# Optimization experiments

Measured on AMD Instinct MI355X. Metric: run time of the kernel, lower is better.

## Reference

```python
import jax, jax.numpy as jnp
import numpy as np

D_MODEL = 1024
N_HEADS = 16
HEAD_DIM = D_MODEL // N_HEADS
D_FF = 4 * D_MODEL
B, T = 2, 2048
EPS = 1e-5


def setup_inputs() -> dict:
    key = jax.random.key(0)
    ks = jax.random.split(key, 12)
    s = 0.02
    x = jax.random.normal(ks[0], (B, T, D_MODEL), dtype=jnp.float32)
    # causal mask: True where attention is disallowed (masked_fill semantics)
    mask = jnp.triu(jnp.ones((T, T), dtype=bool), k=1)[None, None]
    def lin(k, out_d, in_d):
        return jax.random.normal(k, (out_d, in_d), dtype=jnp.float32) * s
    return {
        "x": x,
        "mask": mask,
        "wq_w": lin(ks[1], D_MODEL, D_MODEL), "wq_b": jnp.zeros((D_MODEL,), jnp.float32),
        "wk_w": lin(ks[2], D_MODEL, D_MODEL), "wk_b": jnp.zeros((D_MODEL,), jnp.float32),
        "wv_w": lin(ks[3], D_MODEL, D_MODEL), "wv_b": jnp.zeros((D_MODEL,), jnp.float32),
        "wo_w": lin(ks[4], D_MODEL, D_MODEL), "wo_b": jnp.zeros((D_MODEL,), jnp.float32),
        "fc1_w": lin(ks[5], D_FF, D_MODEL), "fc1_b": jnp.zeros((D_FF,), jnp.float32),
        "fc2_w": lin(ks[6], D_MODEL, D_FF), "fc2_b": jnp.zeros((D_MODEL,), jnp.float32),
        "ln1_g": jnp.ones((D_MODEL,), jnp.float32), "ln1_b": jnp.zeros((D_MODEL,), jnp.float32),
        "ln2_g": jnp.ones((D_MODEL,), jnp.float32), "ln2_b": jnp.zeros((D_MODEL,), jnp.float32),
    }


def _layer_norm(x, g, b):
    mu = jnp.mean(x, axis=-1, keepdims=True)
    var = jnp.mean(jnp.square(x - mu), axis=-1, keepdims=True)
    return (x - mu) * jax.lax.rsqrt(var + EPS) * g + b


def reference(x, mask, wq_w, wq_b, wk_w, wk_b, wv_w, wv_b, wo_w, wo_b,
              fc1_w, fc1_b, fc2_w, fc2_b, ln1_g, ln1_b, ln2_g, ln2_b):
    Bx, Tx, C = x.shape
    # --- attention sub-block (pre-norm) ---
    h = _layer_norm(x, ln1_g, ln1_b)
    q = h @ wq_w.T + wq_b
    k = h @ wk_w.T + wk_b
    v = h @ wv_w.T + wv_b
    # split heads: [B,T,C] -> [B,H,T,Dh]
    def split(t):
        return t.reshape(Bx, Tx, N_HEADS, HEAD_DIM).transpose(0, 2, 1, 3)
    q, k, v = split(q), split(k), split(v)
    scores = jnp.einsum('bhqd,bhkd->bhqk', q, k) / jnp.sqrt(jnp.float32(HEAD_DIM))
    scores = jnp.where(mask, jnp.float32(-1e9), scores)
    attn = jax.nn.softmax(scores, axis=-1)
    ctx = jnp.einsum('bhqk,bhkd->bhqd', attn, v)
    ctx = ctx.transpose(0, 2, 1, 3).reshape(Bx, Tx, C)
    x = x + (ctx @ wo_w.T + wo_b)
    # --- FFN sub-block (pre-norm) ---
    h = _layer_norm(x, ln2_g, ln2_b)
    h = jax.nn.gelu(h @ fc1_w.T + fc1_b, approximate=False)
    x = x + (h @ fc2_w.T + fc2_b)
    return x
```

## Files before the change

### kernel.cpp

```cpp
#include <hip/hip_runtime.h>
#include <stdint.h>

typedef unsigned short u16;
typedef __bf16 bf16x8 __attribute__((ext_vector_type(8)));
typedef float floatx4 __attribute__((ext_vector_type(4)));

#define AS1(p) ((__attribute__((address_space(1))) void*)(void*)(p))
#define AS3(p) ((__attribute__((address_space(3))) void*)(p))

__device__ __forceinline__ u16 f2bf(float f) {
    unsigned u;
    __builtin_memcpy(&u, &f, 4);
    u += 0x7FFF + ((u >> 16) & 1);
    return (u16)(u >> 16);
}
__device__ __forceinline__ u16 f2bf_trunc(float f) {
    unsigned u;
    __builtin_memcpy(&u, &f, 4);
    return (u16)(u >> 16);
}
__device__ __forceinline__ float exp2_fast(float x) {
    return __builtin_amdgcn_exp2f(x);
}
__device__ __forceinline__ float gelu_f(float x) {
    return 0.5f * x * (1.0f + erff(x * 0.70710678118654752f));
}

__global__ __launch_bounds__(256) void conv_w_kernel(
    const float* __restrict__ wq, const float* __restrict__ wk,
    const float* __restrict__ wv, const float* __restrict__ wo,
    const float* __restrict__ f1, const float* __restrict__ f2,
    const float* __restrict__ bq, const float* __restrict__ bk,
    const float* __restrict__ bv, float* __restrict__ qkvb,
    u16* __restrict__ W) {
    const size_t i4 = ((size_t)blockIdx.x * 256 + threadIdx.x) * 4;
    const size_t M1 = 1048576;
    const float* src;
    size_t off;
    if (i4 < M1)            { src = wq; off = i4; }
    else if (i4 < 2 * M1)   { src = wk; off = i4 - M1; }
    else if (i4 < 3 * M1)   { src = wv; off = i4 - 2 * M1; }
    else if (i4 < 4 * M1)   { src = wo; off = i4 - 3 * M1; }
    else if (i4 < 8 * M1)   { src = f1; off = i4 - 4 * M1; }
    else                    { src = f2; off = i4 - 8 * M1; }
    float4 d = *(const float4*)(src + off);
    ushort4 o;
    o.x = f2bf(d.x); o.y = f2bf(d.y); o.z = f2bf(d.z); o.w = f2bf(d.w);
    *(ushort4*)(W + i4) = o;
    if (blockIdx.x == 0) {
        for (int i = threadIdx.x; i < 1024; i += 256) {
            qkvb[i] = bq[i];
            qkvb[1024 + i] = bk[i];
            qkvb[2048 + i] = bv[i];
        }
    }
}

__global__ __launch_bounds__(64) void ln_kernel(const float* __restrict__ X,
                                                const float* __restrict__ G,
                                                const float* __restrict__ Bt,
                                                u16* __restrict__ Y) {
    const int row = blockIdx.x;
    const int lane = threadIdx.x;
    const float* xr = X + (size_t)row * 1024;
    float v[16];
    float s = 0.f;
#pragma unroll
    for (int i = 0; i < 16; ++i) { v[i] = xr[lane + i * 64]; s += v[i]; }
#pragma unroll
    for (int off = 1; off < 64; off <<= 1) s += __shfl_xor(s, off, 64);
    const float mu = s * (1.0f / 1024.0f);
    float ss = 0.f;
#pragma unroll
    for (int i = 0; i < 16; ++i) { float d = v[i] - mu; ss += d * d; }
#pragma unroll
    for (int off = 1; off < 64; off <<= 1) ss += __shfl_xor(ss, off, 64);
    const float rstd = rsqrtf(ss * (1.0f / 1024.0f) + 1e-5f);
    u16* yr = Y + (size_t)row * 1024;
#pragma unroll
    for (int i = 0; i < 16; ++i) {
        int c = lane + i * 64;
        yr[c] = f2bf((v[i] - mu) * rstd * G[c] + Bt[c]);
    }
}

__global__ __launch_bounds__(256, 3) void gemm128_kernel(
    const u16* __restrict__ A, const u16* __restrict__ Bt,
    const float* __restrict__ bias, const float* __restrict__ resid,
    float* __restrict__ C, int M, int N, int K) {
    __shared__ __align__(16) u16 lA[2 * 128 * 64];
    __shared__ __align__(16) u16 lB[2 * 64 * 64];
    const int tid = threadIdx.x;
    const int wave = tid >> 6, lane = tid & 63;
    const int wm = (wave >> 1) * 64;
    const int wn = (wave & 1) * 32;
    const int lr = lane & 15, lk8 = (lane >> 4) * 8;
    const int r0 = (lane >> 4) * 4;
    const int m0 = blockIdx.x * 128, n0 = blockIdx.y * 64;
    const int NT = K >> 6;
    const u16* const Ab = A + (size_t)m0 * K;
    const u16* const Bb = Bt + (size_t)n0 * K;

    const int srow = tid >> 3;
    const int scol = 8 * ((tid & 7) ^ (srow & 7));
    const int sdst = tid * 8;
    const int swz = (lr & 7) << 3;
    const int c0 = lk8 ^ swz;
    const int c1 = (32 + lk8) ^ swz;

    floatx4 acc[4][2];
#pragma unroll
    for (int i = 0; i < 4; ++i)
#pragma unroll
        for (int j = 0; j < 2; ++j) acc[i][j] = floatx4{0.f, 0.f, 0.f, 0.f};
    bf16x8 aF[4][2], bF[2][2];

#define STAGE128(Pb, Tt)                                                       \
    {                                                                          \
        _Pragma("unroll")                                                      \
        for (int l = 0; l < 4; ++l) {                                          \
            const u16* srcA = Ab + (size_t)(l * 32 + srow) * K +               \
                              (size_t)(Tt) * 64 + scol;                        \
            __builtin_amdgcn_global_load_lds(                                  \
                AS1(srcA), AS3(lA + (Pb) * 8192 + l * 2048 + sdst), 16, 0, 0); \
        }                                                                      \
        _Pragma("unroll")                                                      \
        for (int l = 0; l < 2; ++l) {                                          \
            const u16* srcB = Bb + (size_t)(l * 32 + srow) * K +               \
                              (size_t)(Tt) * 64 + scol;                        \
            __builtin_amdgcn_global_load_lds(                                  \
                AS1(srcB), AS3(lB + (Pb) * 4096 + l * 2048 + sdst), 16, 0, 0); \
        }                                                                      \
    }
#define GROUP128(P, T)                                                         \
    {                                                                          \
        if ((T) + 1 < NT) {                                                    \
            STAGE128((P) ^ 1, (T) + 1);                                        \
            asm volatile("s_waitcnt vmcnt(6)" ::: "memory");                   \
        } else {                                                               \
            asm volatile("s_waitcnt vmcnt(0)" ::: "memory");                   \
        }                                                                      \
        asm volatile("s_barrier" ::: "memory");                                \
        _Pragma("unroll")                                                      \
        for (int i = 0; i < 4; ++i) {                                          \
            aF[i][0] = *(const bf16x8*)&lA[(P) * 8192 + (wm + i * 16 + lr) * 64 + c0]; \
            aF[i][1] = *(const bf16x8*)&lA[(P) * 8192 + (wm + i * 16 + lr) * 64 + c1]; \
        }                                                                      \
        _Pragma("unroll")                                                      \
        for (int j = 0; j < 2; ++j) {                                          \
            bF[j][0] = *(const bf16x8*)&lB[(P) * 4096 + (wn + j * 16 + lr) * 64 + c0]; \
            bF[j][1] = *(const bf16x8*)&lB[(P) * 4096 + (wn + j * 16 + lr) * 64 + c1]; \
        }                                                                      \
        asm volatile("s_waitcnt lgkmcnt(0)" ::: "memory");                     \
        __builtin_amdgcn_sched_barrier(0);                                     \
        __builtin_amdgcn_s_setprio(1);                                         \
        _Pragma("unroll")                                                      \
        for (int i = 0; i < 4; ++i)                                            \
            _Pragma("unroll")                                                  \
            for (int j = 0; j < 2; ++j)                                        \
                _Pragma("unroll")                                              \
                for (int kk = 0; kk < 2; ++kk)                                 \
                    acc[i][j] = __builtin_amdgcn_mfma_f32_16x16x32_bf16(       \
                        aF[i][kk], bF[j][kk], acc[i][j], 0, 0, 0);             \
        __builtin_amdgcn_s_setprio(0);                                         \
        asm volatile("s_barrier" ::: "memory");                                \
    }

    STAGE128(0, 0);
    for (int T = 0; T < NT; T += 2) {
        GROUP128(0, T);
        GROUP128(1, T + 1);
    }
#undef GROUP128
#undef STAGE128

#pragma unroll
    for (int i = 0; i < 4; ++i)
#pragma unroll
        for (int j = 0; j < 2; ++j) {
            const int col = n0 + wn + j * 16 + lr;
            const float bv = bias[col];
#pragma unroll
            for (int r = 0; r < 4; ++r) {
                const int row = m0 + wm + i * 16 + r0 + r;
                C[(size_t)row * N + col] =
                    acc[i][j][r] + bv + resid[(size_t)row * N + col];
            }
        }
}

__global__ __launch_bounds__(512, 2) void gemm256_kernel(
    const u16* __restrict__ A, const u16* __restrict__ Bt,
    const float* __restrict__ bias, u16* __restrict__ C,
    int M, int N, int K, int act) {
    extern __shared__ __align__(16) u16 smem[];
    u16* const lA = smem;
    u16* const lB = smem + 32768;
    const int tid = threadIdx.x;
    const int wave = tid >> 6, lane = tid & 63;
    const int wm = (wave >> 2) * 128;
    const int wn = (wave & 3) * 64;
    const int lr = lane & 15, lk8 = (lane >> 4) * 8;
    const int r0 = (lane >> 4) * 4;

    const int gM = M >> 8;
    int bid = blockIdx.x;
    { const int nwg = gridDim.x;
      const int q = nwg >> 3, r = nwg & 7, xcd = bid & 7, lid = bid >> 3;
      bid = (xcd < r ? xcd * (q + 1) : r * (q + 1) + (xcd - r) * q) + lid; }
    const int m0 = (bid % gM) << 8;
    const int n0 = (bid / gM) << 8;

    const int NT = K >> 6;
    const u16* const Ab = A + (size_t)m0 * K;
    const u16* const Bb = Bt + (size_t)n0 * K;

    const int srow = tid >> 3;
    const int scol = 8 * ((tid & 7) ^ (srow & 7));
    const int sdst = tid * 8;
    const int swz = (lr & 7) << 3;
    const int c0 = lk8 ^ swz;
    const int c1 = (32 + lk8) ^ swz;

    floatx4 acc[8][4];
#pragma unroll
    for (int i = 0; i < 8; ++i)
#pragma unroll
        for (int j = 0; j < 4; ++j) acc[i][j] = floatx4{0.f, 0.f, 0.f, 0.f};
    bf16x8 aF[2][4][2];
    bf16x8 bF[4][2];

#define STAGE_HT(ldsbuf, gbase, h, Tt)                                         \
    {                                                                          \
        _Pragma("unroll")                                                      \
        for (int l = 0; l < 2; ++l) {                                          \
            const u16* src = (gbase) + (size_t)((h) * 128 + l * 64 + srow) * K \
                             + (size_t)(Tt) * 64 + scol;                       \
            __builtin_amdgcn_global_load_lds(                                  \
                AS1(src), AS3((ldsbuf) + (h) * 8192 + l * 4096 + sdst), 16, 0, 0); \
        }                                                                      \
    }
#define PH_BAR() asm volatile("s_barrier" ::: "memory")
#define LGKM0()                                                                \
    do { asm volatile("s_waitcnt lgkmcnt(0)" ::: "memory");                    \
         __builtin_amdgcn_sched_barrier(0); } while (0)
#define MFMA_Q(mq, nq)                                                         \
    __builtin_amdgcn_s_setprio(1);                                             \
    _Pragma("unroll")                                                          \
    for (int i = 0; i < 4; ++i)                                                \
        _Pragma("unroll")                                                      \
        for (int j = 0; j < 2; ++j)                                            \
            _Pragma("unroll")                                                  \
            for (int kk = 0; kk < 2; ++kk)                                     \
                acc[(mq) * 4 + i][(nq) * 2 + j] =                              \
                    __builtin_amdgcn_mfma_f32_16x16x32_bf16(                   \
                        aF[mq][i][kk], bF[(nq) * 2 + j][kk],                   \
                        acc[(mq) * 4 + i][(nq) * 2 + j], 0, 0, 0);             \
    __builtin_amdgcn_s_setprio(0);

#define GROUP(P, T)                                                            \
    {                                                                          \
        u16* const lAp = lA + (P) * 16384;                                     \
        u16* const lBp = lB + (P) * 16384;                                     \
        u16* const lBn = lB + ((P) ^ 1) * 16384;                               \
                                                                  \
        _Pragma("unroll")                                                      \
        for (int i = 0; i < 4; ++i) {                                          \
            aF[0][i][0] = *(const bf16x8*)&lAp[(wm + i * 16 + lr) * 64 + c0];  \
            aF[0][i][1] = *(const bf16x8*)&lAp[(wm + i * 16 + lr) * 64 + c1];  \
        }                                                                      \
        _Pragma("unroll")                                                      \
        for (int nf = 0; nf < 4; ++nf) {                                       \
            bF[nf][0] = *(const bf16x8*)&lBp[(wn + nf * 16 + lr) * 64 + c0];   \
            bF[nf][1] = *(const bf16x8*)&lBp[(wn + nf * 16 + lr) * 64 + c1];   \
        }                                                                      \
        if ((T) + 1 < NT) STAGE_HT(lBn, Bb, 0, (T) + 1);                       \
        PH_BAR(); LGKM0();                                                     \
        MFMA_Q(0, 0);                                                          \
        PH_BAR();                                                              \
                                                                  \
        _Pragma("unroll")                                                      \
        for (int i = 0; i < 4; ++i) {                                          \
            aF[1][i][0] = *(const bf16x8*)&lAp[(wm + 64 + i * 16 + lr) * 64 + c0]; \
            aF[1][i][1] = *(const bf16x8*)&lAp[(wm + 64 + i * 16 + lr) * 64 + c1]; \
        }                                                                      \
        if ((T) + 1 < NT) STAGE_HT(lBn, Bb, 1, (T) + 1);                       \
        PH_BAR(); LGKM0();                                                     \
        MFMA_Q(0, 1);                                                          \
        PH_BAR();                                                              \
             \
        if ((T) + 2 < NT) STAGE_HT(lAp, Ab, 0, (T) + 2);                       \
        MFMA_Q(1, 0);                                                          \
                                                                  \
        if ((T) + 2 < NT) STAGE_HT(lAp, Ab, 1, (T) + 2);                       \
        MFMA_Q(1, 1);                                                          \
        if ((T) + 2 < NT) asm volatile("s_waitcnt vmcnt(4)" ::: "memory");     \
        else              asm volatile("s_waitcnt vmcnt(0)" ::: "memory");     \
        PH_BAR();                                                              \
    }

    STAGE_HT(lA, Ab, 0, 0);
    STAGE_HT(lA, Ab, 1, 0);
    STAGE_HT(lB, Bb, 0, 0);
    STAGE_HT(lB, Bb, 1, 0);
    if (NT > 1) {
        STAGE_HT(lA + 16384, Ab, 0, 1);
        STAGE_HT(lA + 16384, Ab, 1, 1);
    }
    asm volatile("s_waitcnt vmcnt(4)" ::: "memory");
    PH_BAR();

    for (int T = 0; T < NT; T += 2) {
        GROUP(0, T);
        GROUP(1, T + 1);
    }
#undef GROUP
#undef MFMA_Q
#undef LGKM0
#undef PH_BAR
#undef STAGE_HT

#pragma unroll
    for (int mq = 0; mq < 2; ++mq)
#pragma unroll
        for (int i = 0; i < 4; ++i)
#pragma unroll
            for (int nf = 0; nf < 4; ++nf) {
                const int col = n0 + wn + nf * 16 + lr;
                const float bv = bias[col];
                floatx4 v = acc[mq * 4 + i][nf];
#pragma unroll
                for (int r = 0; r < 4; ++r) {
                    const int row = m0 + wm + mq * 64 + i * 16 + r0 + r;
                    float x = v[r] + bv;
                    if (act) x = gelu_f(x);
                    C[(size_t)row * N + col] = f2bf(x);
                }
            }
}

__global__ __launch_bounds__(256) void transp_v(const u16* __restrict__ qkv,
                                                u16* __restrict__ vT) {
    __shared__ u16 lT[64 * 64];
    const int bh = blockIdx.x, tt = blockIdx.y;
    const int b = bh >> 4, h = bh & 15;
    const int t0 = tt * 64;
    const int tid = threadIdx.x;
    const int srow = tid >> 3, scol = (tid & 7) * 8;
#pragma unroll
    for (int rr = 0; rr < 2; ++rr) {
        const int row = srow + rr * 32;
        uint4 d4 = *(const uint4*)(qkv + (size_t)(b * 2048 + t0 + row) * 3072 +
                                   2048 + h * 64 + scol);
        const u16* e = (const u16*)&d4;
#pragma unroll
        for (int t = 0; t < 8; ++t) lT[(scol + t) * 64 + row] = e[t];
    }
    __syncthreads();
#pragma unroll
    for (int rr = 0; rr < 2; ++rr) {
        const int row = srow + rr * 32;
        uint4 d4 = *(const uint4*)&lT[row * 64 + scol];
        *(uint4*)(vT + (size_t)(bh * 64 + row) * 2048 + t0 + scol) = d4;
    }
}

__global__ __launch_bounds__(256) void attn_kernel(const u16* __restrict__ qkv,
                                                   const u16* __restrict__ vT,
                                                   u16* __restrict__ O) {
    __shared__ __align__(16) u16 lK[2][64 * 64];
    __shared__ __align__(16) u16 lV[2][64 * 64];
    __shared__ __align__(16) u16 lP[4][16 * 64];
    const int tid = threadIdx.x;
    const int wave = tid >> 6, lane = tid & 63;
    const int lr = lane & 15, khi = lane >> 4, lk8 = khi * 8;
    const int p = blockIdx.x;
    const int bh = blockIdx.y;
    const int b = bh >> 4, hh = bh & 15;
    const int rb = b * 2048;
    const size_t vbase = (size_t)(bh * 64) * 2048;
    const int r0 = khi * 4;
    const int qa = 31 - p, qb = p;
    const int qa0 = qa * 64, qb0 = qb * 64;
    const float C = 0.125f * 1.44269504088896f;

    const int srow = tid >> 3;
    const int scol = 8 * ((tid & 7) ^ (srow & 7));
    const int sdst = tid * 8;
    const int swz = (lr & 7) << 3;
    const int cc0 = lk8 ^ swz;
    const int cc1 = (32 + lk8) ^ swz;

    bf16x8 aqA0, aqA1, aqB0, aqB1;
    {
        const size_t qoffA = (size_t)(rb + qa0 + wave * 16 + lr) * 3072 + hh * 64;
        aqA0 = *(const bf16x8*)(qkv + qoffA + lk8);
        aqA1 = *(const bf16x8*)(qkv + qoffA + 32 + lk8);
        const size_t qoffB = (size_t)(rb + qb0 + wave * 16 + lr) * 3072 + hh * 64;
        aqB0 = *(const bf16x8*)(qkv + qoffB + lk8);
        aqB1 = *(const bf16x8*)(qkv + qoffB + 32 + lk8);
    }

    floatx4 oA[4], oB[4];
    float lA_[4], lB_[4];
#pragma unroll
    for (int r = 0; r < 4; ++r) {
        oA[r] = floatx4{0.f, 0.f, 0.f, 0.f};
        oB[r] = floatx4{0.f, 0.f, 0.f, 0.f};
        lA_[r] = 0.f; lB_[r] = 0.f;
    }

#define ASTAGE(Pb, kt_)                                                        \
    {                                                                          \
        const int k0_ = (kt_) * 64;                                            \
        _Pragma("unroll")                                                      \
        for (int rr = 0; rr < 2; ++rr) {                                       \
            const int row = srow + rr * 32;                                    \
            __builtin_amdgcn_global_load_lds(                                  \
                AS1(qkv + (size_t)(rb + k0_ + row) * 3072 + 1024 + hh * 64 + scol), \
                AS3(lK[Pb] + rr * 2048 + sdst), 16, 0, 0);                     \
            __builtin_amdgcn_global_load_lds(                                  \
                AS1(vT + vbase + (size_t)row * 2048 + k0_ + scol),             \
                AS3(lV[Pb] + rr * 2048 + sdst), 16, 0, 0);                     \
        }                                                                      \
    }

#define TILE_ROUND(Pb, aq0_, aq1_, oo_, ll_, q0_, diag_, k0_)                   \
    {                                                                           \
        float s[4][4];                                                          \
        __builtin_amdgcn_s_setprio(1);                                          \
        _Pragma("unroll")                                                       \
        for (int j = 0; j < 4; ++j) {                                           \
            bf16x8 bk0 = *(const bf16x8*)&lK[Pb][(j * 16 + lr) * 64 + cc0];     \
            bf16x8 bk1 = *(const bf16x8*)&lK[Pb][(j * 16 + lr) * 64 + cc1];     \
            floatx4 t = floatx4{0.f, 0.f, 0.f, 0.f};                            \
            t = __builtin_amdgcn_mfma_f32_16x16x32_bf16(aq0_, bk0, t, 0, 0, 0); \
            t = __builtin_amdgcn_mfma_f32_16x16x32_bf16(aq1_, bk1, t, 0, 0, 0); \
            _Pragma("unroll")                                                   \
            for (int r = 0; r < 4; ++r) s[j][r] = t[r];                         \
        }                                                                       \
        __builtin_amdgcn_s_setprio(0);                                          \
        if (diag_) {                                                            \
            _Pragma("unroll")                                                   \
            for (int j = 0; j < 4; ++j)                                         \
                _Pragma("unroll")                                               \
                for (int r = 0; r < 4; ++r)                                     \
                    if ((k0_) + j * 16 + lr > (q0_) + wave * 16 + r0 + r)       \
                        s[j][r] = -1e30f;                                       \
        }                                                                       \
        _Pragma("unroll")                                                       \
        for (int j = 0; j < 4; ++j)                                             \
            _Pragma("unroll")                                                   \
            for (int r = 0; r < 4; ++r) {                                       \
                float pv = exp2_fast(s[j][r] * C);                              \
                ll_[r] += pv;                                                   \
                lP[wave][(r0 + r) * 64 +                                        \
                         ((j * 16 + lr) ^ (((r0 + r) & 7) << 3))] =             \
                    f2bf_trunc(pv);                                             \
            }                                                                   \
        bf16x8 ap0 = *(const bf16x8*)&lP[wave][lr * 64 + cc0];                  \
        bf16x8 ap1 = *(const bf16x8*)&lP[wave][lr * 64 + cc1];                  \
        __builtin_amdgcn_s_setprio(1);                                          \
        _Pragma("unroll")                                                       \
        for (int jd = 0; jd < 4; ++jd) {                                        \
            bf16x8 bv0 = *(const bf16x8*)&lV[Pb][(jd * 16 + lr) * 64 + cc0];    \
            bf16x8 bv1 = *(const bf16x8*)&lV[Pb][(jd * 16 + lr) * 64 + cc1];    \
            oo_[jd] = __builtin_amdgcn_mfma_f32_16x16x32_bf16(ap0, bv0, oo_[jd], 0, 0, 0); \
            oo_[jd] = __builtin_amdgcn_mfma_f32_16x16x32_bf16(ap1, bv1, oo_[jd], 0, 0, 0); \
        }                                                                       \
        __builtin_amdgcn_s_setprio(0);                                          \
    }

    ASTAGE(0, 0);
    for (int kt = 0; kt <= qa; ++kt) {
        const int P = kt & 1;
        const int k0 = kt * 64;
        if (kt < qa) {
            ASTAGE(P ^ 1, kt + 1);
            asm volatile("s_waitcnt vmcnt(4)" ::: "memory");
        } else {
            asm volatile("s_waitcnt vmcnt(0)" ::: "memory");
        }
        asm volatile("s_barrier" ::: "memory");

        TILE_ROUND(P, aqA0, aqA1, oA, lA_, qa0, kt == qa, k0);
        if (kt <= qb)
            TILE_ROUND(P, aqB0, aqB1, oB, lB_, qb0, kt == qb, k0);

        asm volatile("s_barrier" ::: "memory");
    }
#undef TILE_ROUND
#undef ASTAGE

#pragma unroll
    for (int off = 1; off < 16; off <<= 1)
#pragma unroll
        for (int r = 0; r < 4; ++r) {
            lA_[r] += __shfl_xor(lA_[r], off, 64);
            lB_[r] += __shfl_xor(lB_[r], off, 64);
        }

#pragma unroll
    for (int r = 0; r < 4; ++r) {
        const float invA = 1.0f / lA_[r];
        const float invB = 1.0f / lB_[r];
#pragma unroll
        for (int jd = 0; jd < 4; ++jd) {
            const size_t offA = (size_t)(rb + qa0 + wave * 16 + r0 + r) * 1024 +
                                hh * 64 + jd * 16 + lr;
            O[offA] = f2bf(oA[jd][r] * invA);
            const size_t offB = (size_t)(rb + qb0 + wave * 16 + r0 + r) * 1024 +
                                hh * 64 + jd * 16 + lr;
            O[offB] = f2bf(oB[jd][r] * invB);
        }
    }
}

extern "C" void kernel_launch(void* const* d_in, const int* in_sizes, int n_in,
                              void* d_out, int out_size, void* d_ws, size_t ws_size,
                              hipStream_t stream) {
    const float* x     = (const float*)d_in[0];
    const float* wq_w  = (const float*)d_in[2];
    const float* wq_b  = (const float*)d_in[3];
    const float* wk_w  = (const float*)d_in[4];
    const float* wk_b  = (const float*)d_in[5];
    const float* wv_w  = (const float*)d_in[6];
    const float* wv_b  = (const float*)d_in[7];
    const float* wo_w  = (const float*)d_in[8];
    const float* wo_b  = (const float*)d_in[9];
    const float* fc1_w = (const float*)d_in[10];
    const float* fc1_b = (const float*)d_in[11];
    const float* fc2_w = (const float*)d_in[12];
    const float* fc2_b = (const float*)d_in[13];
    const float* ln1_g = (const float*)d_in[14];
    const float* ln1_b = (const float*)d_in[15];
    const float* ln2_g = (const float*)d_in[16];
    const float* ln2_b = (const float*)d_in[17];
    float* out = (float*)d_out;

    char* ws = (char*)d_ws;
    const size_t M1 = 1048576;
    const size_t MB = 1048576;
    u16* Wc    = (u16*)ws;
    u16* wqc   = Wc;
    u16* woc   = Wc + 3 * M1;
    u16* f1c   = Wc + 4 * M1;
    u16* f2c   = Wc + 8 * M1;
    u16* h     = (u16*)(ws + 24 * MB);
    u16* ctx   = h;
    u16* qkv   = (u16*)(ws + 32 * MB);
    u16* vT    = (u16*)(ws + 56 * MB);
    u16* ffh   = (u16*)(ws + 32 * MB);
    float* x1  = (float*)(ws + 64 * MB);
    float* qkvb = x1;
    u16* h2    = h;

    const dim3 blk(256);

    static bool s_attr_done = false;
    if (!s_attr_done) {
        hipFuncSetAttribute(reinterpret_cast<const void*>(gemm256_kernel),
                            hipFuncAttributeMaxDynamicSharedMemorySize, 131072);
        s_attr_done = true;
    }

    conv_w_kernel<<<12288, 256, 0, stream>>>(wq_w, wk_w, wv_w, wo_w, fc1_w, fc2_w,
                                             wq_b, wk_b, wv_b, qkvb, Wc);
    ln_kernel<<<4096, 64, 0, stream>>>(x, ln1_g, ln1_b, h);
    gemm256_kernel<<<dim3(16 * 12), dim3(512), 131072, stream>>>(
        h, wqc, qkvb, qkv, 4096, 3072, 1024, 0);
    transp_v<<<dim3(32, 32), blk, 0, stream>>>(qkv, vT);
    attn_kernel<<<dim3(16, 32), blk, 0, stream>>>(qkv, vT, ctx);
    gemm128_kernel<<<dim3(32, 16), blk, 0, stream>>>(
        ctx, woc, wo_b, x, x1, 4096, 1024, 1024);
    ln_kernel<<<4096, 64, 0, stream>>>(x1, ln2_g, ln2_b, h2);
    gemm256_kernel<<<dim3(16 * 16), dim3(512), 131072, stream>>>(
        h2, f1c, fc1_b, ffh, 4096, 4096, 1024, 1);
    gemm128_kernel<<<dim3(32, 16), blk, 0, stream>>>(
        ffh, f2c, fc2_b, x1, out, 4096, 1024, 4096);
}
```

Before: 360.6 us.

## Widen output-projection GEMMs to 128x128 tiles with a 4-stage LDS pipeline

Replaces the 128x64 residual GEMM with a 128x128 tile that keeps four K-stages in dynamic shared memory, so loads are prefetched three iterations ahead and each iteration needs one barrier instead of two. Each wave now computes a 64x64 sub-tile, which raises MFMA work per LDS read. The grid halves to 256 blocks, under one wave of blocks on a 256-CU part, and the 128 KB of LDS with launch bounds of one block per CU lowers occupancy.

```diff
diff --git a/kernel.cpp b/kernel.cpp
--- a/kernel.cpp
+++ b/kernel.cpp
@@ -84,19 +84,18 @@
     }
 }
 
-__global__ __launch_bounds__(256, 3) void gemm128_kernel(
+__global__ __launch_bounds__(256, 1) void gemm128sq_kernel(
     const u16* __restrict__ A, const u16* __restrict__ Bt,
     const float* __restrict__ bias, const float* __restrict__ resid,
     float* __restrict__ C, int M, int N, int K) {
-    __shared__ __align__(16) u16 lA[2 * 128 * 64];
-    __shared__ __align__(16) u16 lB[2 * 64 * 64];
+    extern __shared__ __align__(16) u16 smem[];
     const int tid = threadIdx.x;
     const int wave = tid >> 6, lane = tid & 63;
     const int wm = (wave >> 1) * 64;
-    const int wn = (wave & 1) * 32;
+    const int wn = (wave & 1) * 64;
     const int lr = lane & 15, lk8 = (lane >> 4) * 8;
     const int r0 = (lane >> 4) * 4;
-    const int m0 = blockIdx.x * 128, n0 = blockIdx.y * 64;
+    const int m0 = blockIdx.x * 128, n0 = blockIdx.y * 128;
     const int NT = K >> 6;
     const u16* const Ab = A + (size_t)m0 * K;
     const u16* const Bb = Bt + (size_t)n0 * K;
@@ -108,76 +107,71 @@
     const int c0 = lk8 ^ swz;
     const int c1 = (32 + lk8) ^ swz;
 
-    floatx4 acc[4][2];
+    floatx4 acc[4][4];
 #pragma unroll
     for (int i = 0; i < 4; ++i)
 #pragma unroll
-        for (int j = 0; j < 2; ++j) acc[i][j] = floatx4{0.f, 0.f, 0.f, 0.f};
-    bf16x8 aF[4][2], bF[2][2];
-
-#define STAGE128(Pb, Tt)                                                       \
+        for (int j = 0; j < 4; ++j) acc[i][j] = floatx4{0.f, 0.f, 0.f, 0.f};
+    bf16x8 aF[4][2], bF[4][2];
+
+#define STG(Tt)                                                                \
     {                                                                          \
+        u16* const buf = smem + ((Tt) & 3) * 16384;                            \
         _Pragma("unroll")                                                      \
         for (int l = 0; l < 4; ++l) {                                          \
             const u16* srcA = Ab + (size_t)(l * 32 + srow) * K +               \
                               (size_t)(Tt) * 64 + scol;                        \
             __builtin_amdgcn_global_load_lds(                                  \
-                AS1(srcA), AS3(lA + (Pb) * 8192 + l * 2048 + sdst), 16, 0, 0); \
-        }                                                                      \
-        _Pragma("unroll")                                                      \
-        for (int l = 0; l < 2; ++l) {                                          \
+                AS1(srcA), AS3(buf + l * 2048 + sdst), 16, 0, 0);              \
+        }                                                                      \
+        _Pragma("unroll")                                                      \
+        for (int l = 0; l < 4; ++l) {                                          \
             const u16* srcB = Bb + (size_t)(l * 32 + srow) * K +               \
                               (size_t)(Tt) * 64 + scol;                        \
             __builtin_amdgcn_global_load_lds(                                  \
-                AS1(srcB), AS3(lB + (Pb) * 4096 + l * 2048 + sdst), 16, 0, 0); \
-        }                                                                      \
-    }
-#define GROUP128(P, T)                                                         \
-    {                                                                          \
-        if ((T) + 1 < NT) {                                                    \
-            STAGE128((P) ^ 1, (T) + 1);                                        \
-            asm volatile("s_waitcnt vmcnt(6)" ::: "memory");                   \
-        } else {                                                               \
-            asm volatile("s_waitcnt vmcnt(0)" ::: "memory");                   \
-        }                                                                      \
-        asm volatile("s_barrier" ::: "memory");                                \
-        _Pragma("unroll")                                                      \
-        for (int i = 0; i < 4; ++i) {                                          \
-            aF[i][0] = *(const bf16x8*)&lA[(P) * 8192 + (wm + i * 16 + lr) * 64 + c0]; \
-            aF[i][1] = *(const bf16x8*)&lA[(P) * 8192 + (wm + i * 16 + lr) * 64 + c1]; \
-        }                                                                      \
-        _Pragma("unroll")                                                      \
-        for (int j = 0; j < 2; ++j) {                                          \
-            bF[j][0] = *(const bf16x8*)&lB[(P) * 4096 + (wn + j * 16 + lr) * 64 + c0]; \
-            bF[j][1] = *(const bf16x8*)&lB[(P) * 4096 + (wn + j * 16 + lr) * 64 + c1]; \
-        }                                                                      \
-        asm volatile("s_waitcnt lgkmcnt(0)" ::: "memory");                     \
-        __builtin_amdgcn_sched_barrier(0);                                     \
-        __builtin_amdgcn_s_setprio(1);                                         \
-        _Pragma("unroll")                                                      \
-        for (int i = 0; i < 4; ++i)                                            \
-            _Pragma("unroll")                                                  \
-            for (int j = 0; j < 2; ++j)                                        \
-                _Pragma("unroll")                                              \
-                for (int kk = 0; kk < 2; ++kk)                                 \
-                    acc[i][j] = __builtin_amdgcn_mfma_f32_16x16x32_bf16(       \
-                        aF[i][kk], bF[j][kk], acc[i][j], 0, 0, 0);             \
-        __builtin_amdgcn_s_setprio(0);                                         \
-        asm volatile("s_barrier" ::: "memory");                                \
-    }
-
-    STAGE128(0, 0);
-    for (int T = 0; T < NT; T += 2) {
-        GROUP128(0, T);
-        GROUP128(1, T + 1);
-    }
-#undef GROUP128
-#undef STAGE128
+                AS1(srcB), AS3(buf + 8192 + l * 2048 + sdst), 16, 0, 0);       \
+        }                                                                      \
+    }
+
+    STG(0); STG(1); STG(2);
+    for (int T = 0; T < NT; ++T) {
+        const int rem = NT - 1 - T;
+        if (rem >= 2)      asm volatile("s_waitcnt vmcnt(16)" ::: "memory");
+        else if (rem == 1) asm volatile("s_waitcnt vmcnt(8)" ::: "memory");
+        else               asm volatile("s_waitcnt vmcnt(0)" ::: "memory");
+        asm volatile("s_barrier" ::: "memory");
+        if (T + 3 < NT) STG(T + 3);
+        const u16* const bufA = smem + (T & 3) * 16384;
+        const u16* const bufB = bufA + 8192;
+#pragma unroll
+        for (int i = 0; i < 4; ++i) {
+            aF[i][0] = *(const bf16x8*)&bufA[(wm + i * 16 + lr) * 64 + c0];
+            aF[i][1] = *(const bf16x8*)&bufA[(wm + i * 16 + lr) * 64 + c1];
+        }
+#pragma unroll
+        for (int j = 0; j < 4; ++j) {
+            bF[j][0] = *(const bf16x8*)&bufB[(wn + j * 16 + lr) * 64 + c0];
+            bF[j][1] = *(const bf16x8*)&bufB[(wn + j * 16 + lr) * 64 + c1];
+        }
+        asm volatile("s_waitcnt lgkmcnt(0)" ::: "memory");
+        __builtin_amdgcn_sched_barrier(0);
+        __builtin_amdgcn_s_setprio(1);
+#pragma unroll
+        for (int i = 0; i < 4; ++i)
+#pragma unroll
+            for (int j = 0; j < 4; ++j)
+#pragma unroll
+                for (int kk = 0; kk < 2; ++kk)
+                    acc[i][j] = __builtin_amdgcn_mfma_f32_16x16x32_bf16(
+                        aF[i][kk], bF[j][kk], acc[i][j], 0, 0, 0);
+        __builtin_amdgcn_s_setprio(0);
+    }
+#undef STG
 
 #pragma unroll
     for (int i = 0; i < 4; ++i)
 #pragma unroll
-        for (int j = 0; j < 2; ++j) {
+        for (int j = 0; j < 4; ++j) {
             const int col = n0 + wn + j * 16 + lr;
             const float bv = bias[col];
 #pragma unroll
@@ -561,6 +555,8 @@
     if (!s_attr_done) {
         hipFuncSetAttribute(reinterpret_cast<const void*>(gemm256_kernel),
                             hipFuncAttributeMaxDynamicSharedMemorySize, 131072);
+        hipFuncSetAttribute(reinterpret_cast<const void*>(gemm128sq_kernel),
+                            hipFuncAttributeMaxDynamicSharedMemorySize, 131072);
         s_attr_done = true;
     }
 
@@ -571,11 +567,11 @@
         h, wqc, qkvb, qkv, 4096, 3072, 1024, 0);
     transp_v<<<dim3(32, 32), blk, 0, stream>>>(qkv, vT);
     attn_kernel<<<dim3(16, 32), blk, 0, stream>>>(qkv, vT, ctx);
-    gemm128_kernel<<<dim3(32, 16), blk, 0, stream>>>(
+    gemm128sq_kernel<<<dim3(32, 8), blk, 131072, stream>>>(
         ctx, woc, wo_b, x, x1, 4096, 1024, 1024);
     ln_kernel<<<4096, 64, 0, stream>>>(x1, ln2_g, ln2_b, h2);
     gemm256_kernel<<<dim3(16 * 16), dim3(512), 131072, stream>>>(
         h2, f1c, fc1_b, ffh, 4096, 4096, 1024, 1);
-    gemm128_kernel<<<dim3(32, 16), blk, 0, stream>>>(
+    gemm128sq_kernel<<<dim3(32, 8), blk, 131072, stream>>>(
         ffh, f2c, fc2_b, x1, out, 4096, 1024, 4096);
 }
```

Result: slower. 381.1 us (+5.7%).
